# Performance work log

Measured on AMD Instinct MI355X. Metric: run time of the kernel, lower is better.

The kernel has to match this reference:

```python
import jax, jax.numpy as jnp
import numpy as np

N = 2_000_000
REL_DIM = 14
CAN_DIM = 64
N_TYPES = 4


def setup_inputs() -> dict:
    key = jax.random.key(0)
    ka, kb, kia, kib, kw, kbias = jax.random.split(key, 6)
    return {
        "relation_logits_a": jax.random.normal(ka, (N, REL_DIM), dtype=jnp.float32),
        "relation_logits_b": jax.random.normal(kb, (N, REL_DIM), dtype=jnp.float32),
        "frame_type_ids_a": jax.random.randint(kia, (N,), 0, N_TYPES, dtype=jnp.int32),
        "frame_type_ids_b": jax.random.randint(kib, (N,), 0, N_TYPES, dtype=jnp.int32),
        # stacked expert params: W[e] is (REL_DIM, CAN_DIM), b[e] is (CAN_DIM,)
        "W": jax.random.normal(kw, (N_TYPES, REL_DIM, CAN_DIM), dtype=jnp.float32) * 0.26,
        "b": jax.random.normal(kbias, (N_TYPES, CAN_DIM), dtype=jnp.float32) * 0.26,
    }


def _batch_project(x, ids, W, b):
    # x: (N, REL_DIM), ids: (N,) int in [0, N_TYPES)
    # Masked dispatch to 4 tiny linear experts; peak intermediate is (N, CAN_DIM).
    out = jnp.zeros((x.shape[0], CAN_DIM), dtype=x.dtype)
    for e in range(N_TYPES):
        y = x @ W[e] + b[e]                      # (N, CAN_DIM)
        out = out + jnp.where((ids == e)[:, None], y, jnp.zeros((), x.dtype))
    return out


def reference(relation_logits_a, relation_logits_b, frame_type_ids_a, frame_type_ids_b, W, b):
    proj_a = _batch_project(relation_logits_a, frame_type_ids_a, W, b)
    proj_b = _batch_project(relation_logits_b, frame_type_ids_b, W, b)
    # F.mse_loss default reduction='mean'
    diff = proj_a - proj_b
    return jnp.mean(diff * diff)
```

## Files before the change

### kernel.cpp

```cpp
#include <hip/hip_runtime.h>
#include <hip/hip_fp16.h>


#define N_ROWS   2000000
#define N_CHUNKS (N_ROWS / 64)
#define NBLK     4096
#define LDSW     36

typedef _Float16     h8 __attribute__((ext_vector_type(8)));
typedef float        f4 __attribute__((ext_vector_type(4)));
typedef unsigned int u4 __attribute__((ext_vector_type(4)));
typedef unsigned int u2 __attribute__((ext_vector_type(2)));

__device__ __forceinline__ unsigned int pkrtz(float a, float b) {
    return __builtin_bit_cast(unsigned int, __builtin_amdgcn_cvt_pkrtz(a, b));
}

struct RawRegs {
    u4 a4[3]; u2 a2;
    u4 b4[3]; u2 b2;
    int ea, eb;
};

__device__ __forceinline__ RawRegs load_chunk(int c, int lane,
        const float* __restrict__ A, const float* __restrict__ B,
        const int* __restrict__ IDA, const int* __restrict__ IDB) {
    RawRegs r;
    const char* pa = (const char*)A + (size_t)c * 3584;
    const char* pb = (const char*)B + (size_t)c * 3584;
#pragma unroll
    for (int j = 0; j < 3; ++j) {
        r.a4[j] = *(const u4*)(pa + j * 1024 + lane * 16);
        r.b4[j] = *(const u4*)(pb + j * 1024 + lane * 16);
    }
    r.a2 = *(const u2*)(pa + 3072 + lane * 8);
    r.b2 = *(const u2*)(pb + 3072 + lane * 8);
    r.ea = IDA[c * 64 + lane];
    r.eb = IDB[c * 64 + lane];
    return r;
}

__device__ __forceinline__ void stage_write(unsigned int* __restrict__ s, int lane,
                                            const RawRegs& r) {
#pragma unroll
    for (int j = 0; j < 3; ++j) {
        *(u4*)(s +       j * 256 + lane * 4) = r.a4[j];
        *(u4*)(s + 896 + j * 256 + lane * 4) = r.b4[j];
    }
    *(u2*)(s +       768 + lane * 2) = r.a2;
    *(u2*)(s + 896 + 768 + lane * 2) = r.b2;
}

__device__ __forceinline__ void pack_scatter(unsigned int* __restrict__ s, int lane,
                                             int ea, int eb) {
    const float* sa = (const float*)s + 14 * lane;
    const float* sb = (const float*)s + 896 + 14 * lane;
    unsigned int pa[7], pb[7];
    const bool same = (ea == eb);
#pragma unroll
    for (int t = 0; t < 7; ++t) {
        float2 av = *(const float2*)(sa + 2 * t);
        float2 bv = *(const float2*)(sb + 2 * t);
        float sx = same ? (av.x - bv.x) : av.x;
        float sy = same ? (av.y - bv.y) : av.y;
        pa[t] = pkrtz(sx, sy);
        pb[t] = pkrtz(-bv.x, -bv.y);
    }
    unsigned int* row32 = s + lane * LDSW;
    const u4 z = {0u, 0u, 0u, 0u};
#pragma unroll
    for (int t = 0; t < 8; ++t) ((u4*)row32)[t] = z;
#pragma unroll
    for (int t = 0; t < 7; ++t) row32[7 * ea + t] = pa[t];
    if (!same) {
#pragma unroll
        for (int t = 0; t < 7; ++t) row32[7 * eb + t] = pb[t];
        const unsigned wa = 0x3C00u << ((ea & 1) * 16);
        const unsigned wb = 0xBC00u << ((eb & 1) * 16);
        const int ja = 28 + (ea >> 1), jb = 28 + (eb >> 1);
        if (ja == jb) row32[ja] = wa | wb;
        else { row32[ja] = wa; row32[jb] = wb; }
    }
}

__device__ __forceinline__ void compute_chunk(const unsigned int* __restrict__ sbuf,
                                              int sub, int quad, const h8* wf,
                                              float* ls) {
#pragma unroll
    for (int t = 0; t < 4; ++t) {
        const unsigned int* fr = sbuf + (t * 16 + sub) * LDSW + quad * 4;
        u4 lo = *(const u4*)fr;
        u4 hi = *(const u4*)(fr + 16);
        const h8 e0 = __builtin_bit_cast(h8, lo);
        const h8 e1 = __builtin_bit_cast(h8, hi);
#pragma unroll
        for (int ct = 0; ct < 4; ++ct) {
            const f4 z = {0.0f, 0.0f, 0.0f, 0.0f};
            f4 acc = __builtin_amdgcn_mfma_f32_16x16x32_f16(e0, wf[ct * 2 + 0], z, 0, 0, 0);
            acc     = __builtin_amdgcn_mfma_f32_16x16x32_f16(e1, wf[ct * 2 + 1], acc, 0, 0, 0);
#pragma unroll
            for (int rr = 0; rr < 4; ++rr)
                ls[rr] = fmaf(acc[rr], acc[rr], ls[rr]);
        }
    }
}

__global__ void __launch_bounds__(64, 4)
frame_loss(const float* __restrict__ A, const float* __restrict__ B,
           const int* __restrict__ IDA, const int* __restrict__ IDB,
           const float* __restrict__ W, const float* __restrict__ BIAS,
           float* __restrict__ ws)
{
    __shared__ alignas(16) unsigned int s0[64 * LDSW];

    const int lane = threadIdx.x;
    const int sub  = lane & 15;
    const int quad = lane >> 4;

    h8 wf[8];
#pragma unroll
    for (int ct = 0; ct < 4; ++ct)
#pragma unroll
        for (int s = 0; s < 2; ++s) {
            h8 f;
            const int c = ct * 16 + sub;
#pragma unroll
            for (int j = 0; j < 8; ++j) {
                const int k = s * 32 + quad * 8 + j;
                float v = 0.0f;
                if (k < 56)       v = W[k * 64 + c];
                else if (k < 60)  v = BIAS[(k - 56) * 64 + c];
                f[j] = (_Float16)v;
            }
            wf[ct * 2 + s] = f;
        }

    float ls[4] = {0.0f, 0.0f, 0.0f, 0.0f};
    const int stride = gridDim.x;

    int c = blockIdx.x;
    RawRegs rr = load_chunk(c, lane, A, B, IDA, IDB);
    stage_write(s0, lane, rr);
    pack_scatter(s0, lane, rr.ea, rr.eb);

    while (true) {
        int n = c + stride;
        bool more = (n < N_CHUNKS);
        if (more) rr = load_chunk(n, lane, A, B, IDA, IDB);
        compute_chunk(s0, sub, quad, wf, ls);
        if (!more) break;
        stage_write(s0, lane, rr);
        pack_scatter(s0, lane, rr.ea, rr.eb);
        c = n;
    }

    float lsum = ls[0] + ls[1] + ls[2] + ls[3];
#pragma unroll
    for (int off = 32; off > 0; off >>= 1)
        lsum += __shfl_down(lsum, off, 64);
    if (lane == 0)
        ws[blockIdx.x] = lsum;
}

__global__ void __launch_bounds__(256)
reduce_partials(const float* __restrict__ ws, float* __restrict__ out, int nblk)
{
    const int tid = threadIdx.x;
    float s = 0.0f;
    for (int i = tid; i < nblk; i += 256) s += ws[i];
#pragma unroll
    for (int off = 32; off > 0; off >>= 1)
        s += __shfl_down(s, off, 64);
    __shared__ float tmp[4];
    if ((tid & 63) == 0) tmp[tid >> 6] = s;
    __syncthreads();
    if (tid == 0)
        out[0] = (tmp[0] + tmp[1] + tmp[2] + tmp[3]) * (1.0f / 128000000.0f);
}

extern "C" void kernel_launch(void* const* d_in, const int* in_sizes, int n_in,
                              void* d_out, int out_size, void* d_ws, size_t ws_size,
                              hipStream_t stream) {
    const float* A    = (const float*)d_in[0];
    const float* B    = (const float*)d_in[1];
    const int*   IDA  = (const int*)d_in[2];
    const int*   IDB  = (const int*)d_in[3];
    const float* W    = (const float*)d_in[4];
    const float* BIAS = (const float*)d_in[5];
    float* ws  = (float*)d_ws;
    float* out = (float*)d_out;

    const int nblk = (ws_size >= (size_t)NBLK * sizeof(float)) ? NBLK : 2048;

    frame_loss<<<dim3(nblk), dim3(64), 0, stream>>>(A, B, IDA, IDB, W, BIAS, ws);
    reduce_partials<<<dim3(1), dim3(256), 0, stream>>>(ws, out, nblk);
}
```

Before: 282.7 us.

## Stage input chunks via direct global-to-LDS DMA with separate pack region

Replaces register-staged global loads plus LDS stores with global_load_lds direct transfers into a raw staging region. The packed fp16 rows move to a separate LDS region, so the next chunk's DMA can be issued right after packing and overlap with the MFMA compute. The aim is to cut VGPR use and the LDS write instructions. The grid shrinks to 2560 blocks and launch bounds drop to 2 waves per EU to match the larger LDS footprint. There is a risk in relying on vmcnt waits for LDS DMA completion and in having fewer waves resident.

```diff
diff --git a/kernel.cpp b/kernel.cpp
--- a/kernel.cpp
+++ b/kernel.cpp
@@ -4,57 +4,42 @@
 
 #define N_ROWS   2000000
 #define N_CHUNKS (N_ROWS / 64)
-#define NBLK     4096
+#define NBLK     2560
 #define LDSW     36
+#define P_OFF    1792
 
 typedef _Float16     h8 __attribute__((ext_vector_type(8)));
 typedef float        f4 __attribute__((ext_vector_type(4)));
 typedef unsigned int u4 __attribute__((ext_vector_type(4)));
-typedef unsigned int u2 __attribute__((ext_vector_type(2)));
+
+typedef __attribute__((address_space(3))) unsigned int       lds_u32;
+typedef __attribute__((address_space(1))) const unsigned int glb_u32;
 
 __device__ __forceinline__ unsigned int pkrtz(float a, float b) {
     return __builtin_bit_cast(unsigned int, __builtin_amdgcn_cvt_pkrtz(a, b));
 }
 
-struct RawRegs {
-    u4 a4[3]; u2 a2;
-    u4 b4[3]; u2 b2;
-    int ea, eb;
-};
-
-__device__ __forceinline__ RawRegs load_chunk(int c, int lane,
-        const float* __restrict__ A, const float* __restrict__ B,
-        const int* __restrict__ IDA, const int* __restrict__ IDB) {
-    RawRegs r;
-    const char* pa = (const char*)A + (size_t)c * 3584;
-    const char* pb = (const char*)B + (size_t)c * 3584;
-#pragma unroll
-    for (int j = 0; j < 3; ++j) {
-        r.a4[j] = *(const u4*)(pa + j * 1024 + lane * 16);
-        r.b4[j] = *(const u4*)(pb + j * 1024 + lane * 16);
-    }
-    r.a2 = *(const u2*)(pa + 3072 + lane * 8);
-    r.b2 = *(const u2*)(pb + 3072 + lane * 8);
-    r.ea = IDA[c * 64 + lane];
-    r.eb = IDB[c * 64 + lane];
-    return r;
+__device__ __forceinline__ void dma16(const void* g, unsigned int* l) {
+    __builtin_amdgcn_global_load_lds((const glb_u32*)g, (lds_u32*)l, 16, 0, 0);
 }
 
-__device__ __forceinline__ void stage_write(unsigned int* __restrict__ s, int lane,
-                                            const RawRegs& r) {
+__device__ __forceinline__ void dma_chunk(unsigned int* S, int lane,
+                                          const char* pa, const char* pb) {
 #pragma unroll
-    for (int j = 0; j < 3; ++j) {
-        *(u4*)(s +       j * 256 + lane * 4) = r.a4[j];
-        *(u4*)(s + 896 + j * 256 + lane * 4) = r.b4[j];
-    }
-    *(u2*)(s +       768 + lane * 2) = r.a2;
-    *(u2*)(s + 896 + 768 + lane * 2) = r.b2;
+    for (int j = 0; j < 3; ++j)
+        dma16(pa + j * 1024 + lane * 16, S + j * 256);
+    const char* gm = (lane < 32) ? (pa + 3072 + lane * 16)
+                                 : (pb + (lane - 32) * 16);
+    dma16(gm, S + 768);
+#pragma unroll
+    for (int j = 0; j < 3; ++j)
+        dma16(pb + 512 + j * 1024 + lane * 16, S + 1024 + j * 256);
 }
 
-__device__ __forceinline__ void pack_scatter(unsigned int* __restrict__ s, int lane,
+__device__ __forceinline__ void pack_scatter(unsigned int* __restrict__ S, int lane,
                                              int ea, int eb) {
-    const float* sa = (const float*)s + 14 * lane;
-    const float* sb = (const float*)s + 896 + 14 * lane;
+    const float* sa = (const float*)S + 14 * lane;
+    const float* sb = (const float*)S + 896 + 14 * lane;
     unsigned int pa[7], pb[7];
     const bool same = (ea == eb);
 #pragma unroll
@@ -66,7 +51,7 @@
         pa[t] = pkrtz(sx, sy);
         pb[t] = pkrtz(-bv.x, -bv.y);
     }
-    unsigned int* row32 = s + lane * LDSW;
+    unsigned int* row32 = S + P_OFF + lane * LDSW;
     const u4 z = {0u, 0u, 0u, 0u};
 #pragma unroll
     for (int t = 0; t < 8; ++t) ((u4*)row32)[t] = z;
@@ -83,12 +68,12 @@
     }
 }
 
-__device__ __forceinline__ void compute_chunk(const unsigned int* __restrict__ sbuf,
+__device__ __forceinline__ void compute_chunk(const unsigned int* __restrict__ S,
                                               int sub, int quad, const h8* wf,
                                               float* ls) {
 #pragma unroll
     for (int t = 0; t < 4; ++t) {
-        const unsigned int* fr = sbuf + (t * 16 + sub) * LDSW + quad * 4;
+        const unsigned int* fr = S + P_OFF + (t * 16 + sub) * LDSW + quad * 4;
         u4 lo = *(const u4*)fr;
         u4 hi = *(const u4*)(fr + 16);
         const h8 e0 = __builtin_bit_cast(h8, lo);
@@ -105,13 +90,13 @@
     }
 }
 
-__global__ void __launch_bounds__(64, 4)
+__global__ void __launch_bounds__(64, 2)
 frame_loss(const float* __restrict__ A, const float* __restrict__ B,
            const int* __restrict__ IDA, const int* __restrict__ IDB,
            const float* __restrict__ W, const float* __restrict__ BIAS,
            float* __restrict__ ws)
 {
-    __shared__ alignas(16) unsigned int s0[64 * LDSW];
+    __shared__ alignas(16) unsigned int S[4096];
 
     const int lane = threadIdx.x;
     const int sub  = lane & 15;
@@ -137,21 +122,35 @@
 
     float ls[4] = {0.0f, 0.0f, 0.0f, 0.0f};
     const int stride = gridDim.x;
+    const char* Ac = (const char*)A;
+    const char* Bc = (const char*)B;
 
     int c = blockIdx.x;
-    RawRegs rr = load_chunk(c, lane, A, B, IDA, IDB);
-    stage_write(s0, lane, rr);
-    pack_scatter(s0, lane, rr.ea, rr.eb);
+    dma_chunk(S, lane, Ac + (size_t)c * 3584, Bc + (size_t)c * 3584);
+    int ea = IDA[c * 64 + lane];
+    int eb = IDB[c * 64 + lane];
+    asm volatile("s_waitcnt vmcnt(0)" ::: "memory");
+    pack_scatter(S, lane, ea, eb);
+
+    int n = c + stride;
+    bool more = (n < N_CHUNKS);
+    if (more) {
+        dma_chunk(S, lane, Ac + (size_t)n * 3584, Bc + (size_t)n * 3584);
+        ea = IDA[n * 64 + lane];
+        eb = IDB[n * 64 + lane];
+    }
 
     while (true) {
-        int n = c + stride;
-        bool more = (n < N_CHUNKS);
-        if (more) rr = load_chunk(n, lane, A, B, IDA, IDB);
-        compute_chunk(s0, sub, quad, wf, ls);
+        compute_chunk(S, sub, quad, wf, ls);
         if (!more) break;
-        stage_write(s0, lane, rr);
-        pack_scatter(s0, lane, rr.ea, rr.eb);
-        c = n;
+        asm volatile("s_waitcnt vmcnt(0)" ::: "memory");
+        pack_scatter(S, lane, ea, eb);
+        c = n; n = c + stride; more = (n < N_CHUNKS);
+        if (more) {
+            dma_chunk(S, lane, Ac + (size_t)n * 3584, Bc + (size_t)n * 3584);
+            ea = IDA[n * 64 + lane];
+            eb = IDB[n * 64 + lane];
+        }
     }
 
     float lsum = ls[0] + ls[1] + ls[2] + ls[3];
```

New measurement: 289.3 us. +2.3%, slower.
